# Performance work log

Measured on AMD Instinct MI355X. Metric: run time of the kernel, lower is better.

Reference implementation:

```python
import jax, jax.numpy as jnp
import numpy as np

N = 100_000      # nodes
E = 1_600_000    # edges (avg degree 16)
H = 4            # heads
C = 32           # per-head channels
HID = 128        # hidden = H*C
L = 4            # layers
IN, ED, OUT = 8, 6, 256
NEG_SLOPE = 0.2  # LeakyReLU default in GATv2Conv


def setup_inputs() -> dict:
    key = jax.random.key(0)
    ks = jax.random.split(key, 16)
    s = 0.1
    return {
        "x": jax.random.normal(ks[0], (N, IN), dtype=jnp.float32),
        "edge_index": jax.random.randint(ks[1], (2, E), 0, N, dtype=jnp.int32),
        "edge_attr": jax.random.normal(ks[2], (E, ED), dtype=jnp.float32),
        "W_in": jax.random.normal(ks[3], (IN, HID), dtype=jnp.float32) * s,
        "b_in": jnp.zeros((HID,), jnp.float32),
        "W_l": jax.random.normal(ks[4], (L, HID, HID), dtype=jnp.float32) * s,
        "b_l": jnp.zeros((L, HID), jnp.float32),
        "W_r": jax.random.normal(ks[5], (L, HID, HID), dtype=jnp.float32) * s,
        "b_r": jnp.zeros((L, HID), jnp.float32),
        "W_e": jax.random.normal(ks[6], (L, ED, HID), dtype=jnp.float32) * s,
        "att": jax.random.normal(ks[7], (L, H, C), dtype=jnp.float32) * s,
        "bias": jnp.zeros((L, HID), jnp.float32),
        "ln_w": jnp.ones((L, HID), jnp.float32),
        "ln_b": jnp.zeros((L, HID), jnp.float32),
        "W_out": jax.random.normal(ks[8], (HID, OUT), dtype=jnp.float32) * s,
        "b_out": jnp.zeros((OUT,), jnp.float32),
    }


def _elu(x):
    return jnp.where(x > 0, x, jnp.expm1(x))


def _leaky(x):
    return jnp.where(x > 0, x, NEG_SLOPE * x)


def _layernorm(x, w, b):
    mu = jnp.mean(x, axis=-1, keepdims=True)
    var = jnp.var(x, axis=-1, keepdims=True)
    return (x - mu) * jax.lax.rsqrt(var + 1e-5) * w + b


def _forward(x, edge_index, edge_attr, W_in, b_in, W_l, b_l, W_r, b_r,
             W_e, att, bias, ln_w, ln_b, W_out, b_out):
    src, dst = edge_index[0], edge_index[1]
    # add_self_loops with fill_value='mean': self-loop edge_attr = mean of incoming edge_attr
    deg = jax.ops.segment_sum(jnp.ones((E,), x.dtype), dst, num_segments=N)
    loop_attr = jax.ops.segment_sum(edge_attr, dst, num_segments=N) / jnp.maximum(deg, 1.0)[:, None]
    loops = jnp.arange(N, dtype=src.dtype)
    src_a = jnp.concatenate([src, loops])          # [E+N]
    dst_a = jnp.concatenate([dst, loops])          # [E+N]
    eattr_a = jnp.concatenate([edge_attr, loop_attr], axis=0)  # [E+N, ED]

    h = _elu(x @ W_in + b_in)  # [N, HID]
    for i in range(L):
        res = h
        xl = (h @ W_l[i] + b_l[i]).reshape(N, H, C)   # source transform
        xr = (h @ W_r[i] + b_r[i]).reshape(N, H, C)   # target transform
        ea = (eattr_a @ W_e[i]).reshape(-1, H, C)     # edge transform
        m = _leaky(xl[src_a] + xr[dst_a] + ea)        # [E+N, H, C]
        score = jnp.einsum('ehc,hc->eh', m, att[i])   # [E+N, H]
        # segment softmax over incoming edges per target node
        smax = jax.ops.segment_max(score, dst_a, num_segments=N)[dst_a]
        ex = jnp.exp(score - smax)
        denom = jax.ops.segment_sum(ex, dst_a, num_segments=N)[dst_a]
        alpha = ex / denom                             # [E+N, H]
        out = jax.ops.segment_sum(alpha[:, :, None] * xl[src_a], dst_a,
                                  num_segments=N).reshape(N, HID) + bias[i]
        h = _elu(_layernorm(out + res, ln_w[i], ln_b[i]))
        # dropout: identity (eval mode)
    return h @ W_out + b_out  # [N, OUT]


def reference(x, edge_index, edge_attr, W_in, b_in, W_l, b_l, W_r, b_r,
              W_e, att, bias, ln_w, ln_b, W_out, b_out):
    return _forward(x, edge_index, edge_attr, W_in, b_in, W_l, b_l, W_r, b_r,
                    W_e, att, bias, ln_w, ln_b, W_out, b_out)
```

## Files before the change

kernel.cpp:

```cpp
#include <hip/hip_runtime.h>
#include <hip/hip_bf16.h>
#include <hip/hip_fp16.h>

#define N_NODES 100000
#define N_EDGES 1600000
#define HEADS 4
#define CHN 32
#define HID 128
#define LAYERS 4
#define IN_F 8
#define ED_F 6
#define OUT_F 256
#define NEG_SLOPE 0.2f

typedef _Float16 f16x8 __attribute__((ext_vector_type(8)));
typedef _Float16 f16x4 __attribute__((ext_vector_type(4)));
typedef _Float16 h2 __attribute__((ext_vector_type(2)));
typedef float f32x4 __attribute__((ext_vector_type(4)));

#if defined(__has_builtin)
#if __has_builtin(__builtin_amdgcn_fdot2)
#define HAVE_FDOT2 1
#endif
#endif

__device__ __forceinline__ float elu_f(float x) {
    return x > 0.f ? x : expm1f(x);
}

__device__ __forceinline__ h2 bith2(float f) {
    union { float f; h2 h; } u; u.f = f; return u.h;
}

__device__ __forceinline__ float dot6(h2 e01, h2 e23, h2 e45, const h2* w) {
#ifdef HAVE_FDOT2
    return __builtin_amdgcn_fdot2(e45, w[2],
           __builtin_amdgcn_fdot2(e23, w[1],
           __builtin_amdgcn_fdot2(e01, w[0], 0.f, false), false), false);
#else
    float s = (float)e01[0] * (float)w[0][0];
    s = fmaf((float)e01[1], (float)w[0][1], s);
    s = fmaf((float)e23[0], (float)w[1][0], s);
    s = fmaf((float)e23[1], (float)w[1][1], s);
    s = fmaf((float)e45[0], (float)w[2][0], s);
    s = fmaf((float)e45[1], (float)w[2][1], s);
    return s;
#endif
}


__global__ void hist_kernel(const int* __restrict__ dst, int* __restrict__ fill) {
    int e = blockIdx.x * blockDim.x + threadIdx.x;
    if (e < N_EDGES) atomicAdd(&fill[dst[e]], 1);
}

__global__ void scan1_kernel(const int* __restrict__ cnt, int* __restrict__ bsum) {
    __shared__ int sd[256];
    int t = threadIdx.x;
    int base = blockIdx.x * 1024 + t * 4;
    int s = 0;
#pragma unroll
    for (int j = 0; j < 4; ++j) {
        int i = base + j;
        if (i < N_NODES) s += cnt[i];
    }
    sd[t] = s;
    for (int off = 128; off > 0; off >>= 1) {
        __syncthreads();
        if (t < off) sd[t] += sd[t + off];
    }
    if (t == 0) bsum[blockIdx.x] = sd[0];
}

__global__ void scan2_kernel(int* __restrict__ bsum, int* __restrict__ rowptr, int nb) {
    int run = 0;
    for (int b = 0; b < nb; ++b) {
        int v = bsum[b];
        bsum[b] = run;
        run += v;
    }
    rowptr[N_NODES] = run;
}

__global__ void scan3_kernel(const int* __restrict__ cnt, const int* __restrict__ bsum,
                             int* __restrict__ rowptr) {
    __shared__ int sd[256];
    int t = threadIdx.x;
    int base = blockIdx.x * 1024 + t * 4;
    int v[4];
#pragma unroll
    for (int j = 0; j < 4; ++j) {
        int i = base + j;
        v[j] = (i < N_NODES) ? cnt[i] : 0;
    }
    int s = v[0] + v[1] + v[2] + v[3];
    sd[t] = s;
    __syncthreads();
    for (int off = 1; off < 256; off <<= 1) {
        int xv = (t >= off) ? sd[t - off] : 0;
        __syncthreads();
        sd[t] += xv;
        __syncthreads();
    }
    int excl = sd[t] - s + bsum[blockIdx.x];
    int pre = 0;
#pragma unroll
    for (int j = 0; j < 4; ++j) {
        int i = base + j;
        if (i < N_NODES) rowptr[i] = excl + pre;
        pre += v[j];
    }
}

__global__ void fill_kernel(const int* __restrict__ src, const int* __restrict__ dst,
                            const int* __restrict__ rowptr, int* __restrict__ fill,
                            int2* __restrict__ csr) {
    int e = blockIdx.x * blockDim.x + threadIdx.x;
    if (e >= N_EDGES) return;
    int d = dst[e];
    int p = rowptr[d] + atomicAdd(&fill[d], 1);
    csr[p] = make_int2(src[e] * (HID * 2), e * 16);
}

__global__ void ecvt_kernel(const float* __restrict__ eattr, __half* __restrict__ ea16) {
    int gid = blockIdx.x * blockDim.x + threadIdx.x;
    if (gid >= N_EDGES * 8) return;
    int e = gid >> 3, d = gid & 7;
    float v = (d < ED_F) ? eattr[e * ED_F + d] : 0.f;
    ea16[gid] = __float2half_rn(v);
}

__global__ void lattr_kernel(const int* __restrict__ rowptr, const int2* __restrict__ csr,
                             const float* __restrict__ eattr, __half* __restrict__ lat16) {
    int gid = blockIdx.x * blockDim.x + threadIdx.x;
    if (gid >= N_NODES * 8) return;
    int n = gid >> 3;
    int d = gid & 7;
    float s = 0.f;
    if (d < ED_F) {
        int rp0 = rowptr[n], rp1 = rowptr[n + 1];
        for (int p = rp0; p < rp1; ++p) {
            int eid = csr[p].y >> 4;
            s += eattr[(size_t)eid * ED_F + d];
        }
        int deg = rp1 - rp0;
        s /= (float)(deg > 0 ? deg : 1);
    }
    lat16[gid] = __float2half_rn(s);
}


__global__ void convw_kernel(const float* __restrict__ W_l, const float* __restrict__ W_r,
                             const float* __restrict__ W_out, __half* __restrict__ wbt) {
    int gid = blockIdx.x * blockDim.x + threadIdx.x;
    if (gid >= 5 * 256 * 128) return;
    int b = gid >> 15;
    int idx = gid & 32767;
    int n = idx >> 7, k = idx & 127;
    float val;
    if (b < 4)
        val = (n < HID) ? W_l[b * HID * HID + k * HID + n]
                        : W_r[b * HID * HID + k * HID + (n - HID)];
    else
        val = W_out[k * OUT_F + n];
    int boff = n * 256 + ((k * 2) ^ ((n & 7) << 4));
    *(__half*)((char*)wbt + (size_t)b * 65536 + boff) = __float2half_rn(val);
}


__global__ void in_kernel(const float* __restrict__ x, const float* __restrict__ Wi,
                          const float* __restrict__ bi, float* __restrict__ h0) {
    int gid = blockIdx.x * blockDim.x + threadIdx.x;
    if (gid >= N_NODES * HID) return;
    int n = gid >> 7, j = gid & 127;
    float acc = bi[j];
#pragma unroll
    for (int k = 0; k < IN_F; ++k) acc = fmaf(x[n * IN_F + k], Wi[k * HID + j], acc);
    h0[gid] = elu_f(acc);
}


#define LDS_B_OFF 16384

template <int MODE>
__global__ __launch_bounds__(256, 2) void gemm_kernel(
    const float* __restrict__ A, const __half* __restrict__ Bt,
    const float* __restrict__ bias0, const float* __restrict__ bias1,
    __half* __restrict__ xl16, float* __restrict__ xr_out, float* __restrict__ outp) {
    __shared__ __align__(16) unsigned char smem[81920];
    int t = threadIdx.x;
    int row0 = blockIdx.x * 64;

#pragma unroll
    for (int it = 0; it < 8; ++it) {
        int idx = it * 256 + t;
        int r = idx >> 5;
        int k4 = (idx & 31) << 2;
        float4 hv = *(const float4*)(A + (size_t)(row0 + r) * HID + k4);
        f16x4 p;
        p[0] = (_Float16)hv.x; p[1] = (_Float16)hv.y;
        p[2] = (_Float16)hv.z; p[3] = (_Float16)hv.w;
        *(f16x4*)(smem + r * 256 + ((k4 * 2) ^ ((r & 7) << 4))) = p;
    }
#pragma unroll
    for (int it = 0; it < 16; ++it) {
        int off = (it * 256 + t) * 16;
        *(float4*)(smem + LDS_B_OFF + off) = *(const float4*)((const char*)Bt + off);
    }
    __syncthreads();

    int wave = t >> 6;
    int lane = t & 63;
    int lc = lane & 15, lr = lane >> 4;
    int cbase = wave * 64;

    f32x4 acc[4][4];
#pragma unroll
    for (int i = 0; i < 4; ++i)
#pragma unroll
        for (int j = 0; j < 4; ++j) acc[i][j] = (f32x4){0.f, 0.f, 0.f, 0.f};

#pragma unroll
    for (int kk = 0; kk < 4; ++kk) {
        int kb = kk * 64 + lr * 16;
        f16x8 av[4], bv[4];
#pragma unroll
        for (int rt = 0; rt < 4; ++rt) {
            int r = rt * 16 + lc;
            av[rt] = *(const f16x8*)(smem + r * 256 + (kb ^ ((r & 7) << 4)));
        }
#pragma unroll
        for (int ct = 0; ct < 4; ++ct) {
            int c = cbase + ct * 16 + lc;
            bv[ct] = *(const f16x8*)(smem + LDS_B_OFF + c * 256 + (kb ^ ((c & 7) << 4)));
        }
#pragma unroll
        for (int rt = 0; rt < 4; ++rt)
#pragma unroll
            for (int ct = 0; ct < 4; ++ct)
                acc[rt][ct] = __builtin_amdgcn_mfma_f32_16x16x32_f16(av[rt], bv[ct],
                                                                     acc[rt][ct], 0, 0, 0);
    }

#pragma unroll
    for (int ct = 0; ct < 4; ++ct) {
        int col = cbase + ct * 16 + lc;
        float bv;
        if (MODE == 0) bv = (col < HID) ? bias0[col] : bias1[col - HID];
        else bv = bias0[col];
#pragma unroll
        for (int rt = 0; rt < 4; ++rt) {
#pragma unroll
            for (int q = 0; q < 4; ++q) {
                int node = row0 + rt * 16 + lr * 4 + q;
                if (node < N_NODES) {
                    float val = acc[rt][ct][q] + bv;
                    if (MODE == 0) {
                        if (col < HID)
                            xl16[(size_t)node * HID + col] = __float2half_rn(val);
                        else
                            xr_out[(size_t)node * HID + (col - HID)] = val;
                    } else {
                        outp[(size_t)node * OUT_F + col] = val;
                    }
                }
            }
        }
    }
}


struct Slot {
    float4 er;
    float2 xv;
};

__device__ __forceinline__ void slot_issue(Slot& s, int i, int total, int rp0,
                                           const int2* __restrict__ csr,
                                           const char* eab, const char* lat16v,
                                           const char* xlb, int vbytes) {
    i = min(i, total - 1);
    const char* eb;
    const char* xb;
    if (i == 0) {
        eb = lat16v;
        xb = xlb + (size_t)vbytes;
    } else {
        int2 se = csr[rp0 + i - 1];
        eb = eab + (size_t)se.y;
        xb = xlb + (size_t)se.x;
    }
    s.er = *(const float4*)eb;
    s.xv = *(const float2*)xb;
}

__device__ __forceinline__ void slot_consume(const Slot& sl, int i, int total,
                                             const h2 we_h2[4][3], const float* attv,
                                             const float* xrv,
                                             float& denom, float* acc) {
    h2 e01 = bith2(sl.er.x), e23 = bith2(sl.er.y), e45 = bith2(sl.er.z);
    h2 x01 = bith2(sl.xv.x), x23 = bith2(sl.xv.y);
    float xf[4];
    xf[0] = (float)x01[0]; xf[1] = (float)x01[1];
    xf[2] = (float)x23[0]; xf[3] = (float)x23[1];
    float t = 0.f;
#pragma unroll
    for (int c = 0; c < 4; ++c) {
        float ea = dot6(e01, e23, e45, we_h2[c]);
        float m = xf[c] + xrv[c] + ea;
        m = m > 0.f ? m : NEG_SLOPE * m;
        t = fmaf(m, attv[c], t);
    }
    t += __shfl_xor(t, 1);
    t += __shfl_xor(t, 2);
    t += __shfl_xor(t, 4);
    float ex = __expf(t);
    ex = (i < total) ? ex : 0.f;
    denom += ex;
#pragma unroll
    for (int c = 0; c < 4; ++c) acc[c] = fmaf(ex, xf[c], acc[c]);
}

__global__ __launch_bounds__(64, 8) void edge_kernel(
    const __half* __restrict__ xl, const float* __restrict__ xr,
    const float* __restrict__ hcur, float* __restrict__ hnext,
    const int* __restrict__ rowptr, const int2* __restrict__ csr,
    const __half* __restrict__ ea16, const __half* __restrict__ lat16,
    const float* __restrict__ We, const float* __restrict__ att,
    const float* __restrict__ bias_l, const float* __restrict__ lnw,
    const float* __restrict__ lnb) {
    int v = blockIdx.x;
    int lane = threadIdx.x;
    int half = lane >> 5;
    int hl = lane & 31;
    int c0 = hl * 4;

    h2 we_h2[4][3];
#pragma unroll
    for (int c = 0; c < 4; ++c)
#pragma unroll
        for (int d = 0; d < 3; ++d) {
            h2 w;
            w[0] = (_Float16)We[(2 * d) * HID + c0 + c];
            w[1] = (_Float16)We[(2 * d + 1) * HID + c0 + c];
            we_h2[c][d] = w;
        }
    float4 at4 = *(const float4*)(att + c0);
    float attv[4] = {at4.x, at4.y, at4.z, at4.w};
    float4 xr4 = *(const float4*)(xr + (size_t)v * HID + c0);
    float xrv[4] = {xr4.x, xr4.y, xr4.z, xr4.w};

    int rp0 = rowptr[v], rp1 = rowptr[v + 1];
    int total = (rp1 - rp0) + 1;
    int R = (total + 1) >> 1;

    const char* xlb = (const char*)xl + (size_t)c0 * 2;
    const char* eab = (const char*)ea16;
    const char* lat16v = (const char*)lat16 + (size_t)v * 16;
    int vbytes = v * (HID * 2);

    float denom = 0.f;
    float acc[4] = {0.f, 0.f, 0.f, 0.f};

    Slot sA, sB;
    slot_issue(sA, half, total, rp0, csr, eab, lat16v, xlb, vbytes);
    if (R > 1) slot_issue(sB, 2 + half, total, rp0, csr, eab, lat16v, xlb, vbytes);
    int r = 0;
    for (; r + 2 <= R; r += 2) {
        slot_consume(sA, 2 * r + half, total, we_h2, attv, xrv, denom, acc);
        if (r + 2 < R) slot_issue(sA, 2 * (r + 2) + half, total, rp0, csr, eab, lat16v, xlb, vbytes);
        slot_consume(sB, 2 * (r + 1) + half, total, we_h2, attv, xrv, denom, acc);
        if (r + 3 < R) slot_issue(sB, 2 * (r + 3) + half, total, rp0, csr, eab, lat16v, xlb, vbytes);
    }
    if (r < R) slot_consume(sA, 2 * r + half, total, we_h2, attv, xrv, denom, acc);

    denom += __shfl_xor(denom, 32);
#pragma unroll
    for (int c = 0; c < 4; ++c) acc[c] += __shfl_xor(acc[c], 32);

    float rd = 1.f / denom;

    float4 res4 = *(const float4*)(hcur + (size_t)v * HID + c0);
    float4 bv4 = *(const float4*)(bias_l + c0);
    float y[4];
    y[0] = acc[0] * rd + bv4.x + res4.x;
    y[1] = acc[1] * rd + bv4.y + res4.y;
    y[2] = acc[2] * rd + bv4.z + res4.z;
    y[3] = acc[3] * rd + bv4.w + res4.w;
    float s = y[0] + y[1] + y[2] + y[3];
    float sq = fmaf(y[0], y[0], fmaf(y[1], y[1], fmaf(y[2], y[2], y[3] * y[3])));
#pragma unroll
    for (int off = 1; off < 32; off <<= 1) {
        s += __shfl_xor(s, off);
        sq += __shfl_xor(sq, off);
    }
    float mu = s * (1.f / HID);
    float var = sq * (1.f / HID) - mu * mu;
    float rstd = rsqrtf(var + 1e-5f);
    float4 wv4 = *(const float4*)(lnw + c0);
    float4 lb4 = *(const float4*)(lnb + c0);
    if (half == 0) {
        float4 o;
        o.x = elu_f((y[0] - mu) * rstd * wv4.x + lb4.x);
        o.y = elu_f((y[1] - mu) * rstd * wv4.y + lb4.y);
        o.z = elu_f((y[2] - mu) * rstd * wv4.z + lb4.z);
        o.w = elu_f((y[3] - mu) * rstd * wv4.w + lb4.w);
        *(float4*)(hnext + (size_t)v * HID + c0) = o;
    }
}


extern "C" void kernel_launch(void* const* d_in, const int* in_sizes, int n_in,
                              void* d_out, int out_size, void* d_ws, size_t ws_size,
                              hipStream_t stream) {
    const float* x     = (const float*)d_in[0];
    const int*   ei    = (const int*)d_in[1];
    const float* eattr = (const float*)d_in[2];
    const float* W_in  = (const float*)d_in[3];
    const float* b_in  = (const float*)d_in[4];
    const float* W_l   = (const float*)d_in[5];
    const float* b_l   = (const float*)d_in[6];
    const float* W_r   = (const float*)d_in[7];
    const float* b_r   = (const float*)d_in[8];
    const float* W_e   = (const float*)d_in[9];
    const float* att   = (const float*)d_in[10];
    const float* bias  = (const float*)d_in[11];
    const float* lnw   = (const float*)d_in[12];
    const float* lnb   = (const float*)d_in[13];
    const float* W_out = (const float*)d_in[14];
    const float* b_out = (const float*)d_in[15];
    float* out = (float*)d_out;

    float* h0    = (float*)d_ws;
    float* h1    = h0 + (size_t)N_NODES * HID;
    __half* lat16 = (__half*)(h1 + (size_t)N_NODES * HID);
    int* rowptr  = (int*)(lat16 + (size_t)N_NODES * 8);
    int* fill    = rowptr + (N_NODES + 1);
    int2* csr    = (int2*)(fill + N_NODES);
    int* bsum    = (int*)(csr + N_EDGES);
    __half* wbt  = (__half*)(bsum + 128);

    float*  xr   = out;
    __half* xl   = (__half*)(out + (size_t)N_NODES * HID);
    __half* ea16 = xl + (size_t)N_NODES * HID;

    const int* srcv = ei;
    const int* dstv = ei + N_EDGES;

    hipMemsetAsync(fill, 0, N_NODES * sizeof(int), stream);
    hist_kernel<<<(N_EDGES + 255) / 256, 256, 0, stream>>>(dstv, fill);
    int nb = (N_NODES + 1023) / 1024;
    scan1_kernel<<<nb, 256, 0, stream>>>(fill, bsum);
    scan2_kernel<<<1, 1, 0, stream>>>(bsum, rowptr, nb);
    scan3_kernel<<<nb, 256, 0, stream>>>(fill, bsum, rowptr);
    hipMemsetAsync(fill, 0, N_NODES * sizeof(int), stream);
    fill_kernel<<<(N_EDGES + 255) / 256, 256, 0, stream>>>(srcv, dstv, rowptr, fill, csr);
    ecvt_kernel<<<(N_EDGES * 8 + 255) / 256, 256, 0, stream>>>(eattr, ea16);
    lattr_kernel<<<(N_NODES * 8 + 255) / 256, 256, 0, stream>>>(rowptr, csr, eattr, lat16);

    convw_kernel<<<(5 * 256 * 128 + 255) / 256, 256, 0, stream>>>(W_l, W_r, W_out, wbt);
    in_kernel<<<(N_NODES * HID) / 256, 256, 0, stream>>>(x, W_in, b_in, h0);

    int gemm_grid = (N_NODES + 63) / 64;
    float* hc = h0;
    float* hn = h1;
    for (int l = 0; l < LAYERS; ++l) {
        gemm_kernel<0><<<gemm_grid, 256, 0, stream>>>(
            hc, wbt + (size_t)l * 32768, b_l + (size_t)l * HID, b_r + (size_t)l * HID,
            xl, xr, nullptr);
        edge_kernel<<<N_NODES, 64, 0, stream>>>(
            xl, xr, hc, hn, rowptr, csr, ea16, lat16,
            W_e + (size_t)l * ED_F * HID, att + (size_t)l * HEADS * CHN,
            bias + (size_t)l * HID, lnw + (size_t)l * HID, lnb + (size_t)l * HID);
        float* tmp = hc; hc = hn; hn = tmp;
    }

    gemm_kernel<1><<<gemm_grid, 256, 0, stream>>>(
        hc, wbt + (size_t)4 * 32768, b_out, nullptr, nullptr, nullptr, out);
}
```

Baseline: 1.084 ms.

## Compute GATv2 edge messages in packed fp16 with four edges per wavefront

The edge kernel now gives each lane 8 channels and processes four edges in parallel per 64-lane block instead of two. The edge-attribute projection, message sum and LeakyReLU run in packed half2 math, with LeakyReLU written as 0.6*x + 0.4*|x| folded into fdot2 against the attention vector. Edge attributes are stored duplicated per pair so they load directly as half2, and the h buffer is updated in place, dropping the ping-pong copy. The intent is fewer ALU instructions and shuffles per edge. The cost is lower precision in the score computation and an in-place write to h, which is safe only because each node block reads its own row before writing it.

```diff
diff --git a/kernel.cpp b/kernel.cpp
--- a/kernel.cpp
+++ b/kernel.cpp
@@ -32,19 +32,15 @@
     union { float f; h2 h; } u; u.f = f; return u.h;
 }
 
-__device__ __forceinline__ float dot6(h2 e01, h2 e23, h2 e45, const h2* w) {
+__device__ __forceinline__ h2 absh2(h2 a) {
+    union { h2 h; unsigned int u; } x; x.h = a; x.u &= 0x7FFF7FFFu; return x.h;
+}
+
+__device__ __forceinline__ float fdot2f(h2 a, h2 b, float c) {
 #ifdef HAVE_FDOT2
-    return __builtin_amdgcn_fdot2(e45, w[2],
-           __builtin_amdgcn_fdot2(e23, w[1],
-           __builtin_amdgcn_fdot2(e01, w[0], 0.f, false), false), false);
+    return __builtin_amdgcn_fdot2(a, b, c, false);
 #else
-    float s = (float)e01[0] * (float)w[0][0];
-    s = fmaf((float)e01[1], (float)w[0][1], s);
-    s = fmaf((float)e23[0], (float)w[1][0], s);
-    s = fmaf((float)e23[1], (float)w[1][1], s);
-    s = fmaf((float)e45[0], (float)w[2][0], s);
-    s = fmaf((float)e45[1], (float)w[2][1], s);
-    return s;
+    return fmaf((float)a[1], (float)b[1], fmaf((float)a[0], (float)b[0], c));
 #endif
 }
 
@@ -119,13 +115,13 @@
     if (e >= N_EDGES) return;
     int d = dst[e];
     int p = rowptr[d] + atomicAdd(&fill[d], 1);
-    csr[p] = make_int2(src[e] * (HID * 2), e * 16);
+    csr[p] = make_int2(src[e] * (HID * 2), e * 32);
 }
 
 __global__ void ecvt_kernel(const float* __restrict__ eattr, __half* __restrict__ ea16) {
     int gid = blockIdx.x * blockDim.x + threadIdx.x;
-    if (gid >= N_EDGES * 8) return;
-    int e = gid >> 3, d = gid & 7;
+    if (gid >= N_EDGES * 16) return;
+    int e = gid >> 4, j = gid & 15, d = j >> 1;
     float v = (d < ED_F) ? eattr[e * ED_F + d] : 0.f;
     ea16[gid] = __float2half_rn(v);
 }
@@ -133,14 +129,14 @@
 __global__ void lattr_kernel(const int* __restrict__ rowptr, const int2* __restrict__ csr,
                              const float* __restrict__ eattr, __half* __restrict__ lat16) {
     int gid = blockIdx.x * blockDim.x + threadIdx.x;
-    if (gid >= N_NODES * 8) return;
-    int n = gid >> 3;
-    int d = gid & 7;
+    if (gid >= N_NODES * 16) return;
+    int n = gid >> 4;
+    int d = (gid & 15) >> 1;
     float s = 0.f;
     if (d < ED_F) {
         int rp0 = rowptr[n], rp1 = rowptr[n + 1];
         for (int p = rp0; p < rp1; ++p) {
-            int eid = csr[p].y >> 4;
+            int eid = csr[p].y >> 5;
             s += eattr[(size_t)eid * ED_F + d];
         }
         int deg = rp1 - rp0;
@@ -271,8 +267,9 @@
 
 
 struct Slot {
-    float4 er;
-    float2 xv;
+    float4 er0;
+    float2 er1;
+    float4 xv;
 };
 
 __device__ __forceinline__ void slot_issue(Slot& s, int i, int total, int rp0,
@@ -290,40 +287,47 @@
         eb = eab + (size_t)se.y;
         xb = xlb + (size_t)se.x;
     }
-    s.er = *(const float4*)eb;
-    s.xv = *(const float2*)xb;
+    s.er0 = *(const float4*)eb;
+    s.er1 = *(const float2*)(eb + 16);
+    s.xv = *(const float4*)xb;
 }
 
 __device__ __forceinline__ void slot_consume(const Slot& sl, int i, int total,
-                                             const h2 we_h2[4][3], const float* attv,
-                                             const float* xrv,
-                                             float& denom, float* acc) {
-    h2 e01 = bith2(sl.er.x), e23 = bith2(sl.er.y), e45 = bith2(sl.er.z);
-    h2 x01 = bith2(sl.xv.x), x23 = bith2(sl.xv.y);
-    float xf[4];
-    xf[0] = (float)x01[0]; xf[1] = (float)x01[1];
-    xf[2] = (float)x23[0]; xf[3] = (float)x23[1];
+                                             const h2 w2[6][4], const h2* a06, const h2* a04,
+                                             const h2* xr2, float& denom, float* acc) {
+    h2 es0 = bith2(sl.er0.x), es1 = bith2(sl.er0.y), es2 = bith2(sl.er0.z);
+    h2 es3 = bith2(sl.er0.w), es4 = bith2(sl.er1.x), es5 = bith2(sl.er1.y);
+    h2 xl2[4];
+    xl2[0] = bith2(sl.xv.x); xl2[1] = bith2(sl.xv.y);
+    xl2[2] = bith2(sl.xv.z); xl2[3] = bith2(sl.xv.w);
     float t = 0.f;
 #pragma unroll
-    for (int c = 0; c < 4; ++c) {
-        float ea = dot6(e01, e23, e45, we_h2[c]);
-        float m = xf[c] + xrv[c] + ea;
-        m = m > 0.f ? m : NEG_SLOPE * m;
-        t = fmaf(m, attv[c], t);
+    for (int p = 0; p < 4; ++p) {
+        h2 sp = xl2[p] + xr2[p];
+        sp += es0 * w2[0][p];
+        sp += es1 * w2[1][p];
+        sp += es2 * w2[2][p];
+        sp += es3 * w2[3][p];
+        sp += es4 * w2[4][p];
+        sp += es5 * w2[5][p];
+        t = fdot2f(sp, a06[p], t);
+        t = fdot2f(absh2(sp), a04[p], t);
     }
     t += __shfl_xor(t, 1);
     t += __shfl_xor(t, 2);
-    t += __shfl_xor(t, 4);
     float ex = __expf(t);
     ex = (i < total) ? ex : 0.f;
     denom += ex;
 #pragma unroll
-    for (int c = 0; c < 4; ++c) acc[c] = fmaf(ex, xf[c], acc[c]);
-}
-
-__global__ __launch_bounds__(64, 8) void edge_kernel(
+    for (int p = 0; p < 4; ++p) {
+        acc[2 * p]     = fmaf((float)xl2[p][0], ex, acc[2 * p]);
+        acc[2 * p + 1] = fmaf((float)xl2[p][1], ex, acc[2 * p + 1]);
+    }
+}
+
+__global__ __launch_bounds__(64, 4) void edge_kernel(
     const __half* __restrict__ xl, const float* __restrict__ xr,
-    const float* __restrict__ hcur, float* __restrict__ hnext,
+    float* __restrict__ h,
     const int* __restrict__ rowptr, const int2* __restrict__ csr,
     const __half* __restrict__ ea16, const __half* __restrict__ lat16,
     const float* __restrict__ We, const float* __restrict__ att,
@@ -331,81 +335,110 @@
     const float* __restrict__ lnb) {
     int v = blockIdx.x;
     int lane = threadIdx.x;
-    int half = lane >> 5;
-    int hl = lane & 31;
-    int c0 = hl * 4;
-
-    h2 we_h2[4][3];
-#pragma unroll
-    for (int c = 0; c < 4; ++c)
-#pragma unroll
-        for (int d = 0; d < 3; ++d) {
+    int q = lane >> 4;
+    int ql = lane & 15;
+    int c0 = ql * 8;
+
+    h2 w2[6][4];
+#pragma unroll
+    for (int d = 0; d < 6; ++d)
+#pragma unroll
+        for (int p = 0; p < 4; ++p) {
             h2 w;
-            w[0] = (_Float16)We[(2 * d) * HID + c0 + c];
-            w[1] = (_Float16)We[(2 * d + 1) * HID + c0 + c];
-            we_h2[c][d] = w;
+            w[0] = (_Float16)We[d * HID + c0 + 2 * p];
+            w[1] = (_Float16)We[d * HID + c0 + 2 * p + 1];
+            w2[d][p] = w;
         }
-    float4 at4 = *(const float4*)(att + c0);
-    float attv[4] = {at4.x, at4.y, at4.z, at4.w};
-    float4 xr4 = *(const float4*)(xr + (size_t)v * HID + c0);
-    float xrv[4] = {xr4.x, xr4.y, xr4.z, xr4.w};
+    h2 a06[4], a04[4], xr2[4];
+#pragma unroll
+    for (int p = 0; p < 4; ++p) {
+        float2 a = *(const float2*)(att + c0 + 2 * p);
+        h2 t06, t04;
+        t06[0] = (_Float16)(0.6f * a.x); t06[1] = (_Float16)(0.6f * a.y);
+        t04[0] = (_Float16)(0.4f * a.x); t04[1] = (_Float16)(0.4f * a.y);
+        a06[p] = t06; a04[p] = t04;
+        float2 xrv = *(const float2*)(xr + (size_t)v * HID + c0 + 2 * p);
+        h2 x2;
+        x2[0] = (_Float16)xrv.x; x2[1] = (_Float16)xrv.y;
+        xr2[p] = x2;
+    }
 
     int rp0 = rowptr[v], rp1 = rowptr[v + 1];
     int total = (rp1 - rp0) + 1;
-    int R = (total + 1) >> 1;
+    int R = (total + 3) >> 2;
 
     const char* xlb = (const char*)xl + (size_t)c0 * 2;
     const char* eab = (const char*)ea16;
-    const char* lat16v = (const char*)lat16 + (size_t)v * 16;
+    const char* lat16v = (const char*)lat16 + (size_t)v * 32;
     int vbytes = v * (HID * 2);
 
     float denom = 0.f;
-    float acc[4] = {0.f, 0.f, 0.f, 0.f};
+    float acc[8] = {0.f, 0.f, 0.f, 0.f, 0.f, 0.f, 0.f, 0.f};
 
     Slot sA, sB;
-    slot_issue(sA, half, total, rp0, csr, eab, lat16v, xlb, vbytes);
-    if (R > 1) slot_issue(sB, 2 + half, total, rp0, csr, eab, lat16v, xlb, vbytes);
+    slot_issue(sA, q, total, rp0, csr, eab, lat16v, xlb, vbytes);
+    if (R > 1) slot_issue(sB, 4 + q, total, rp0, csr, eab, lat16v, xlb, vbytes);
     int r = 0;
     for (; r + 2 <= R; r += 2) {
-        slot_consume(sA, 2 * r + half, total, we_h2, attv, xrv, denom, acc);
-        if (r + 2 < R) slot_issue(sA, 2 * (r + 2) + half, total, rp0, csr, eab, lat16v, xlb, vbytes);
-        slot_consume(sB, 2 * (r + 1) + half, total, we_h2, attv, xrv, denom, acc);
-        if (r + 3 < R) slot_issue(sB, 2 * (r + 3) + half, total, rp0, csr, eab, lat16v, xlb, vbytes);
-    }
-    if (r < R) slot_consume(sA, 2 * r + half, total, we_h2, attv, xrv, denom, acc);
-
+        slot_consume(sA, 4 * r + q, total, w2, a06, a04, xr2, denom, acc);
+        if (r + 2 < R) slot_issue(sA, 4 * (r + 2) + q, total, rp0, csr, eab, lat16v, xlb, vbytes);
+        slot_consume(sB, 4 * (r + 1) + q, total, w2, a06, a04, xr2, denom, acc);
+        if (r + 3 < R) slot_issue(sB, 4 * (r + 3) + q, total, rp0, csr, eab, lat16v, xlb, vbytes);
+    }
+    if (r < R) slot_consume(sA, 4 * r + q, total, w2, a06, a04, xr2, denom, acc);
+
+    denom += __shfl_xor(denom, 16);
     denom += __shfl_xor(denom, 32);
 #pragma unroll
-    for (int c = 0; c < 4; ++c) acc[c] += __shfl_xor(acc[c], 32);
-
+    for (int c = 0; c < 8; ++c) {
+        acc[c] += __shfl_xor(acc[c], 16);
+        acc[c] += __shfl_xor(acc[c], 32);
+    }
     float rd = 1.f / denom;
 
-    float4 res4 = *(const float4*)(hcur + (size_t)v * HID + c0);
-    float4 bv4 = *(const float4*)(bias_l + c0);
-    float y[4];
-    y[0] = acc[0] * rd + bv4.x + res4.x;
-    y[1] = acc[1] * rd + bv4.y + res4.y;
-    y[2] = acc[2] * rd + bv4.z + res4.z;
-    y[3] = acc[3] * rd + bv4.w + res4.w;
-    float s = y[0] + y[1] + y[2] + y[3];
-    float sq = fmaf(y[0], y[0], fmaf(y[1], y[1], fmaf(y[2], y[2], y[3] * y[3])));
-#pragma unroll
-    for (int off = 1; off < 32; off <<= 1) {
+    float4 res0 = *(const float4*)(h + (size_t)v * HID + c0);
+    float4 res1 = *(const float4*)(h + (size_t)v * HID + c0 + 4);
+    float4 bv0 = *(const float4*)(bias_l + c0);
+    float4 bv1 = *(const float4*)(bias_l + c0 + 4);
+    float y[8];
+    y[0] = acc[0] * rd + bv0.x + res0.x;
+    y[1] = acc[1] * rd + bv0.y + res0.y;
+    y[2] = acc[2] * rd + bv0.z + res0.z;
+    y[3] = acc[3] * rd + bv0.w + res0.w;
+    y[4] = acc[4] * rd + bv1.x + res1.x;
+    y[5] = acc[5] * rd + bv1.y + res1.y;
+    y[6] = acc[6] * rd + bv1.z + res1.z;
+    y[7] = acc[7] * rd + bv1.w + res1.w;
+    float s = 0.f, sq = 0.f;
+#pragma unroll
+    for (int c = 0; c < 8; ++c) {
+        s += y[c];
+        sq = fmaf(y[c], y[c], sq);
+    }
+#pragma unroll
+    for (int off = 1; off < 16; off <<= 1) {
         s += __shfl_xor(s, off);
         sq += __shfl_xor(sq, off);
     }
     float mu = s * (1.f / HID);
     float var = sq * (1.f / HID) - mu * mu;
     float rstd = rsqrtf(var + 1e-5f);
-    float4 wv4 = *(const float4*)(lnw + c0);
-    float4 lb4 = *(const float4*)(lnb + c0);
-    if (half == 0) {
-        float4 o;
-        o.x = elu_f((y[0] - mu) * rstd * wv4.x + lb4.x);
-        o.y = elu_f((y[1] - mu) * rstd * wv4.y + lb4.y);
-        o.z = elu_f((y[2] - mu) * rstd * wv4.z + lb4.z);
-        o.w = elu_f((y[3] - mu) * rstd * wv4.w + lb4.w);
-        *(float4*)(hnext + (size_t)v * HID + c0) = o;
+    float4 wv0 = *(const float4*)(lnw + c0);
+    float4 wv1 = *(const float4*)(lnw + c0 + 4);
+    float4 lb0 = *(const float4*)(lnb + c0);
+    float4 lb1 = *(const float4*)(lnb + c0 + 4);
+    if (q == 0) {
+        float4 o0, o1;
+        o0.x = elu_f((y[0] - mu) * rstd * wv0.x + lb0.x);
+        o0.y = elu_f((y[1] - mu) * rstd * wv0.y + lb0.y);
+        o0.z = elu_f((y[2] - mu) * rstd * wv0.z + lb0.z);
+        o0.w = elu_f((y[3] - mu) * rstd * wv0.w + lb0.w);
+        o1.x = elu_f((y[4] - mu) * rstd * wv1.x + lb1.x);
+        o1.y = elu_f((y[5] - mu) * rstd * wv1.y + lb1.y);
+        o1.z = elu_f((y[6] - mu) * rstd * wv1.z + lb1.z);
+        o1.w = elu_f((y[7] - mu) * rstd * wv1.w + lb1.w);
+        *(float4*)(h + (size_t)v * HID + c0) = o0;
+        *(float4*)(h + (size_t)v * HID + c0 + 4) = o1;
     }
 }
 
@@ -431,18 +464,17 @@
     const float* b_out = (const float*)d_in[15];
     float* out = (float*)d_out;
 
-    float* h0    = (float*)d_ws;
-    float* h1    = h0 + (size_t)N_NODES * HID;
-    __half* lat16 = (__half*)(h1 + (size_t)N_NODES * HID);
-    int* rowptr  = (int*)(lat16 + (size_t)N_NODES * 8);
-    int* fill    = rowptr + (N_NODES + 1);
-    int2* csr    = (int2*)(fill + N_NODES);
-    int* bsum    = (int*)(csr + N_EDGES);
-    __half* wbt  = (__half*)(bsum + 128);
+    float*  h     = (float*)d_ws;
+    __half* xl    = (__half*)(h + (size_t)N_NODES * HID);
+    __half* lat16 = xl + (size_t)N_NODES * HID;
+    int* rowptr   = (int*)(lat16 + (size_t)N_NODES * 16);
+    int* fill     = rowptr + (N_NODES + 4);
+    int2* csr     = (int2*)(fill + N_NODES);
+    int* bsum     = (int*)(csr + N_EDGES);
+    __half* wbt   = (__half*)(bsum + 128);
 
     float*  xr   = out;
-    __half* xl   = (__half*)(out + (size_t)N_NODES * HID);
-    __half* ea16 = xl + (size_t)N_NODES * HID;
+    __half* ea16 = (__half*)(out + (size_t)N_NODES * HID);
 
     const int* srcv = ei;
     const int* dstv = ei + N_EDGES;
@@ -455,26 +487,23 @@
     scan3_kernel<<<nb, 256, 0, stream>>>(fill, bsum, rowptr);
     hipMemsetAsync(fill, 0, N_NODES * sizeof(int), stream);
     fill_kernel<<<(N_EDGES + 255) / 256, 256, 0, stream>>>(srcv, dstv, rowptr, fill, csr);
-    ecvt_kernel<<<(N_EDGES * 8 + 255) / 256, 256, 0, stream>>>(eattr, ea16);
-    lattr_kernel<<<(N_NODES * 8 + 255) / 256, 256, 0, stream>>>(rowptr, csr, eattr, lat16);
+    ecvt_kernel<<<(N_EDGES * 16 + 255) / 256, 256, 0, stream>>>(eattr, ea16);
+    lattr_kernel<<<(N_NODES * 16 + 255) / 256, 256, 0, stream>>>(rowptr, csr, eattr, lat16);
 
     convw_kernel<<<(5 * 256 * 128 + 255) / 256, 256, 0, stream>>>(W_l, W_r, W_out, wbt);
-    in_kernel<<<(N_NODES * HID) / 256, 256, 0, stream>>>(x, W_in, b_in, h0);
+    in_kernel<<<(N_NODES * HID) / 256, 256, 0, stream>>>(x, W_in, b_in, h);
 
     int gemm_grid = (N_NODES + 63) / 64;
-    float* hc = h0;
-    float* hn = h1;
     for (int l = 0; l < LAYERS; ++l) {
         gemm_kernel<0><<<gemm_grid, 256, 0, stream>>>(
-            hc, wbt + (size_t)l * 32768, b_l + (size_t)l * HID, b_r + (size_t)l * HID,
+            h, wbt + (size_t)l * 32768, b_l + (size_t)l * HID, b_r + (size_t)l * HID,
             xl, xr, nullptr);
         edge_kernel<<<N_NODES, 64, 0, stream>>>(
-            xl, xr, hc, hn, rowptr, csr, ea16, lat16,
+            xl, xr, h, rowptr, csr, ea16, lat16,
             W_e + (size_t)l * ED_F * HID, att + (size_t)l * HEADS * CHN,
             bias + (size_t)l * HID, lnw + (size_t)l * HID, lnb + (size_t)l * HID);
-        float* tmp = hc; hc = hn; hn = tmp;
     }
 
     gemm_kernel<1><<<gemm_grid, 256, 0, stream>>>(
-        hc, wbt + (size_t)4 * 32768, b_out, nullptr, nullptr, nullptr, out);
-}
+        h, wbt + (size_t)4 * 32768, b_out, nullptr, nullptr, nullptr, out);
+}
```

Result: slower. 1.234 ms (+13.8%).
